# Optimization experiments

Hardware: AMD Instinct MI355X
Metric: run time of the kernel (lower is better)

The kernel has to match this reference:

```python
import jax, jax.numpy as jnp
import numpy as np

# SRU config from the module: 3 layers, highway_bias=0, rescale=True, no layer_norm.
# rescale factor from sru package: sqrt(1 + exp(highway_bias)*2)
SCALE_X = (1.0 + np.exp(0.0) * 2.0) ** 0.5

IMG_DIM, T, HID, NCLS, B = 512, 12, 1024, 51, 2048


def _sru_layer(x, W, vc, b):
    # x: (T, B, d_in); W: (d_in, k*d); vc: (2, d) gate-recurrence vectors; b: (2, d) biases
    Tn, Bn, d_in = x.shape
    d = vc.shape[1]
    k = W.shape[1] // d  # 4 if d_in != d else 3
    U = jnp.einsum('tbi,ij->tbj', x, W).reshape(Tn, Bn, k, d)
    u0, u1, u2 = U[:, :, 0], U[:, :, 1], U[:, :, 2]
    resid = U[:, :, 3] if k == 4 else x  # projected residual when dims differ
    vf, vr = vc[0], vc[1]
    bf, br = b[0], b[1]

    def step(c, inp):
        u0t, u1t, u2t, xt = inp
        f = jax.nn.sigmoid(u1t + vf * c + bf)          # forget gate (uses c_{t-1})
        c_new = f * c + (1.0 - f) * u0t                # cell update
        r = jax.nn.sigmoid(u2t + vr * c_new + br)      # reset gate (uses c_t, as in SRU CUDA)
        h = r * jnp.tanh(c_new) + (1.0 - r) * xt * SCALE_X  # highway with rescale
        return c_new, h

    c0 = jnp.zeros((Bn, d), x.dtype)
    c_last, h = jax.lax.scan(step, c0, (u0, u1, u2, resid))
    return h, c_last


def setup_inputs() -> dict:
    key = jax.random.key(0)
    ks = jax.random.split(key, 12)
    inp = {}
    inp['x'] = jax.random.normal(ks[0], (B, T, IMG_DIM), jnp.float32)
    # layer 0: 512 -> 1024, k=4; layers 1,2: 1024 -> 1024, k=3
    inp['W0'] = jax.random.normal(ks[1], (IMG_DIM, 4 * HID), jnp.float32) / np.sqrt(IMG_DIM)
    inp['W1'] = jax.random.normal(ks[2], (HID, 3 * HID), jnp.float32) / np.sqrt(HID)
    inp['W2'] = jax.random.normal(ks[3], (HID, 3 * HID), jnp.float32) / np.sqrt(HID)
    inp['vc0'] = jax.random.normal(ks[4], (2, HID), jnp.float32) * 0.1
    inp['vc1'] = jax.random.normal(ks[5], (2, HID), jnp.float32) * 0.1
    inp['vc2'] = jax.random.normal(ks[6], (2, HID), jnp.float32) * 0.1
    inp['b0'] = jnp.zeros((2, HID), jnp.float32)
    inp['b1'] = jnp.zeros((2, HID), jnp.float32)
    inp['b2'] = jnp.zeros((2, HID), jnp.float32)
    inp['fc_w'] = jax.random.normal(ks[7], (HID, NCLS), jnp.float32) / np.sqrt(HID)
    inp['fc_b'] = jnp.zeros((NCLS,), jnp.float32)
    return inp


def reference(x, W0, W1, W2, vc0, vc1, vc2, b0, b1, b2, fc_w, fc_b):
    h = jnp.transpose(x, (1, 0, 2))  # (T, B, img_dim)
    for W, vc, b in ((W0, vc0, b0), (W1, vc1, b1), (W2, vc2, b2)):
        h, _ = _sru_layer(h, W, vc, b)
    # dropout layers are identity in eval mode
    logits = jnp.einsum('tbh,hc->tbc', h, fc_w) + fc_b  # (T, B, num_class)
    return jnp.mean(logits, axis=0)  # (B, num_class)
```

## Files before the change

### kernel.cpp

```cpp
#include <hip/hip_runtime.h>
#include <math.h>

#define TSTEPS 12
#define BATCH  2048
#define IMG    512
#define HIDN   1024
#define NCLASS 51
#define SCALE_X 1.7320508075688772f

typedef __attribute__((ext_vector_type(8)))  _Float16 f16x8;
typedef __attribute__((ext_vector_type(2)))  _Float16 f16x2;
typedef __attribute__((ext_vector_type(16))) float    f32x16;

__device__ __forceinline__ float sigf(float x) {
    return 1.f / (1.f + __expf(-x));
}

#define VMCNT_IMM(n) (0x0F70 | (n))


template<int TJ, int NCOMP>
__global__ __launch_bounds__(256, 2)
void gemm_sru(const _Float16* __restrict__ A, const _Float16* __restrict__ Bt,
              const _Float16* __restrict__ resid,
              const float* __restrict__ vc, const float* __restrict__ bias,
              _Float16* __restrict__ hout, float* __restrict__ hbar, int K,
              int pcshift) {
    constexpr int BN    = 64 * TJ;
    constexpr int NCH   = BN / NCOMP;
    constexpr int ATILE = 192 * 32;
    constexpr int EPAD  = BN + 8;
    constexpr int EPI   = 96 * EPAD;
    constexpr int HREG  = 96 * NCH;
    constexpr int KTH   = NCH / 16;
    constexpr int PAIRS = NCH / 2;
    constexpr int STG   = 4 * ATILE;
    constexpr int TOT   = STG > (EPI + HREG) ? STG : (EPI + HREG);
    __shared__ __align__(16) _Float16 smem[TOT];

    const int tid  = threadIdx.x;
    const int lane = tid & 63;
    const int w    = tid >> 6;

    const int nbx = gridDim.x;
    const int b   = blockIdx.y * nbx + blockIdx.x;
    const int pc1 = (nbx >> 3) - 1;
    const int xk  = b & 7, s = b >> 3;
    const int bx  = xk + ((s & pc1) << 3);
    const int by  = s >> pcshift;

    const int bm  = by * 192;
    const int KT  = K >> 4;

    const int rt0 = bm >> 5;
    auto stageA = [&](int buf, int k0) {
        const int kt0 = k0 >> 4;
        #pragma unroll
        for (int i = 0; i < 3; ++i) {
            const int L = w * 3 + i, rc = L >> 1, kk = L & 1;
            const _Float16* g = A + ((size_t)(rt0 + rc) * KT + kt0 + kk) * 512 + (lane << 3);
            __builtin_amdgcn_global_load_lds(
                (const __attribute__((address_space(1))) unsigned int*)g,
                (__attribute__((address_space(3))) unsigned int*)(smem + buf * ATILE + L * 512),
                16, 0, 0);
        }
    };

    const int wy32 = (w >> 1) * 3;
    const int wx32 = (w & 1) * TJ;
    const int l5   = lane >> 5;
    const int m32  = lane & 31;

    const _Float16* bglob = Bt + (size_t)(bx * (BN >> 5) + wx32) * KT * 512 + (lane << 3);

    f16x8 bfr[2][2][TJ];
    auto loadB = [&](int k0, int slot) {
        const int kt0 = k0 >> 4;
        #pragma unroll
        for (int ks = 0; ks < 2; ++ks)
            #pragma unroll
            for (int j = 0; j < TJ; ++j)
                bfr[slot][ks][j] = *(const f16x8*)&bglob[((size_t)j * KT + kt0 + ks) * 512];
    };

    f32x16 acc[3][TJ];
    #pragma unroll
    for (int i = 0; i < 3; ++i)
        #pragma unroll
        for (int j = 0; j < TJ; ++j)
            #pragma unroll
            for (int r = 0; r < 16; ++r) acc[i][j][r] = 0.f;

    stageA(0, 0);
    stageA(1, 32);
    loadB(0, 0);

    for (int K0 = 0; K0 < K; K0 += 128) {
        #pragma unroll
        for (int u = 0; u < 4; ++u) {
            const int k0 = K0 + u * 32;
            if (k0 + 32 < K) __builtin_amdgcn_s_waitcnt(VMCNT_IMM(3 + 2 * TJ));
            else             __builtin_amdgcn_s_waitcnt(VMCNT_IMM(2 * TJ));
            __builtin_amdgcn_s_barrier();
            if (k0 + 64 < K) stageA((u + 2) & 3, k0 + 64);
            if (k0 + 32 < K) loadB(k0 + 32, (u + 1) & 1);

            const _Float16* la = smem + u * ATILE;
            #pragma unroll
            for (int ks = 0; ks < 2; ++ks) {
                f16x8 a[3];
                #pragma unroll
                for (int i = 0; i < 3; ++i)
                    a[i] = *(const f16x8*)&la[((wy32 + i) * 2 + ks) * 512 + (lane << 3)];
                #pragma unroll
                for (int i = 0; i < 3; ++i)
                    #pragma unroll
                    for (int j = 0; j < TJ; ++j)
                        acc[i][j] = __builtin_amdgcn_mfma_f32_32x32x16_f16(
                            a[i], bfr[u & 1][ks][j], acc[i][j], 0, 0, 0);
            }
        }
    }

    _Float16 (*uld)[EPAD] = (_Float16 (*)[EPAD])smem;
    _Float16* hreg = smem + EPI;
    const int bl   = tid / PAIRS;
    const int pr   = tid % PAIRS;
    const int gcol = bx * NCH + pr * 2;

    #pragma unroll
    for (int pass = 0; pass < 2; ++pass) {
        __syncthreads();
        if ((w >> 1) == pass) {
            #pragma unroll
            for (int i = 0; i < 3; ++i)
                #pragma unroll
                for (int j = 0; j < TJ; ++j)
                    #pragma unroll
                    for (int r = 0; r < 16; ++r) {
                        const int row = i * 32 + (r & 3) + 8 * (r >> 2) + 4 * l5;
                        uld[row][(wx32 + j) * 32 + m32] = (_Float16)acc[i][j][r];
                    }
        }
        __syncthreads();

        if (tid < 8 * PAIRS) {
            const float2 vf  = *(const float2*)&vc[gcol];
            const float2 vr  = *(const float2*)&vc[HIDN + gcol];
            const float2 bfv = *(const float2*)&bias[gcol];
            const float2 brv = *(const float2*)&bias[HIDN + gcol];
            const int ca = (pr * 2) * NCOMP, cb = (pr * 2 + 1) * NCOMP;

            float c0 = 0.f, c1 = 0.f, s0 = 0.f, s1 = 0.f;
            #pragma unroll
            for (int t = 0; t < TSTEPS; ++t) {
                const int row = bl * 12 + t;
                const float u0a = (float)uld[row][ca + 0];
                const float u1a = (float)uld[row][ca + 1];
                const float u2a = (float)uld[row][ca + 2];
                const float u0b = (float)uld[row][cb + 0];
                const float u1b = (float)uld[row][cb + 1];
                const float u2b = (float)uld[row][cb + 2];
                float xta, xtb;
                if (NCOMP == 4) {
                    xta = (float)uld[row][ca + 3];
                    xtb = (float)uld[row][cb + 3];
                } else {
                    const int grow = bm + pass * 96 + row;
                    const size_t gran = ((size_t)(grow >> 5) * KT + (gcol >> 4)) * 512
                                      + (size_t)((grow & 31) + ((gcol >> 3) & 1) * 32) * 8
                                      + (gcol & 7);
                    const f16x2 xv = *(const f16x2*)&resid[gran];
                    xta = (float)xv[0]; xtb = (float)xv[1];
                }

                const float f0 = sigf(u1a + vf.x * c0 + bfv.x);
                c0 = f0 * c0 + (1.f - f0) * u0a;
                const float r0_ = sigf(u2a + vr.x * c0 + brv.x);
                const float th0 = 2.f * sigf(2.f * c0) - 1.f;
                const float hv0 = r0_ * th0 + (1.f - r0_) * xta * SCALE_X;

                const float f1 = sigf(u1b + vf.y * c1 + bfv.y);
                c1 = f1 * c1 + (1.f - f1) * u0b;
                const float r1_ = sigf(u2b + vr.y * c1 + brv.y);
                const float th1 = 2.f * sigf(2.f * c1) - 1.f;
                const float hv1 = r1_ * th1 + (1.f - r1_) * xtb * SCALE_X;

                if (hout) {
                    const int rtl  = row >> 5;
                    const int ktl  = pr >> 3;
                    const int lloc = (row & 31) + ((pr >> 2) & 1) * 32;
                    f16x2 hv = { (_Float16)hv0, (_Float16)hv1 };
                    *(f16x2*)&hreg[(rtl * KTH + ktl) * 512 + lloc * 8 + (pr & 3) * 2] = hv;
                }
                s0 += hv0; s1 += hv1;
            }
            if (hbar) {
                const int gb = bm / 12 + pass * 8 + bl;
                *(float2*)&hbar[(size_t)gb * HIDN + gcol] =
                    make_float2(s0 * (1.f / TSTEPS), s1 * (1.f / TSTEPS));
            }
        }

        if (hout) {
            __syncthreads();
            const int rtg0 = (bm + pass * 96) >> 5;
            for (int g = tid; g < HREG / 8; g += 256) {
                const int c = g >> 6, l = g & 63;
                const f16x8 v = *(const f16x8*)&hreg[c * 512 + l * 8];
                const int rtl = c / KTH, ktl = c % KTH;
                const size_t gc = (size_t)(rtg0 + rtl) * 64 + bx * KTH + ktl;
                *(f16x8*)&hout[gc * 512 + l * 8] = v;
            }
        }
    }
}

template<int NC>
__global__ __launch_bounds__(256)
void wsplit_t(const float* __restrict__ W, _Float16* __restrict__ Wt, int K) {
    __shared__ _Float16 tile[32][132];
    const int N  = NC * 1024;
    const int KT = K >> 4;
    const int rt = blockIdx.x, kc = blockIdx.y;

    const int nl = threadIdx.x & 31;
    const int kl = threadIdx.x >> 5;
    const int np = rt * 32 + nl;
    const int h  = np / NC, comp = np - h * NC;
    const int n  = comp * 1024 + h;
    #pragma unroll
    for (int kk = 0; kk < 16; ++kk) {
        const int k = kc * 128 + kl * 16 + kk;
        tile[nl][kl * 16 + kk] = (_Float16)W[(size_t)k * N + n];
    }
    __syncthreads();

    #pragma unroll
    for (int p = 0; p < 2; ++p) {
        const int slot = p * 256 + threadIdx.x;
        const int ktl  = slot >> 6, l = slot & 63;
        f16x8 v;
        #pragma unroll
        for (int j = 0; j < 8; ++j)
            v[j] = tile[l & 31][ktl * 16 + ((l >> 5) << 3) + j];
        const int kt = kc * 8 + ktl;
        *(f16x8*)&Wt[((size_t)rt * KT + kt) * 512 + l * 8] = v;
    }
}

__global__ __launch_bounds__(256)
void esplit(const float* __restrict__ src, _Float16* __restrict__ dst) {
    __shared__ _Float16 tile[32][132];
    const int rt = blockIdx.x, kc = blockIdx.y;
    const int kli = threadIdx.x & 31;
    const int rl  = threadIdx.x >> 5;
    #pragma unroll
    for (int rr = 0; rr < 4; ++rr) {
        const int row = rl * 4 + rr;
        const float4 v = *(const float4*)&src[(size_t)(rt * 32 + row) * 512 + kc * 128 + kli * 4];
        tile[row][kli * 4 + 0] = (_Float16)v.x;
        tile[row][kli * 4 + 1] = (_Float16)v.y;
        tile[row][kli * 4 + 2] = (_Float16)v.z;
        tile[row][kli * 4 + 3] = (_Float16)v.w;
    }
    __syncthreads();

    #pragma unroll
    for (int p = 0; p < 2; ++p) {
        const int slot = p * 256 + threadIdx.x;
        const int ktl  = slot >> 6, l = slot & 63;
        f16x8 v;
        #pragma unroll
        for (int j = 0; j < 8; ++j)
            v[j] = tile[l & 31][ktl * 16 + ((l >> 5) << 3) + j];
        const int kt = kc * 8 + ktl;
        *(f16x8*)&dst[((size_t)rt * 32 + kt) * 512 + l * 8] = v;
    }
}

__global__ __launch_bounds__(64)
void final_fc(const float* __restrict__ hbar, const float* __restrict__ fcw,
              const float* __restrict__ fcb, float* __restrict__ out) {
    __shared__ float hrow[HIDN];
    const int b = blockIdx.x;
    for (int i = threadIdx.x; i < HIDN; i += 64)
        hrow[i] = hbar[(size_t)b * HIDN + i];
    __syncthreads();

    const int c = threadIdx.x;
    if (c < NCLASS) {
        float acc = fcb[c];
        #pragma unroll 8
        for (int k = 0; k < HIDN; ++k)
            acc = fmaf(hrow[k], fcw[(size_t)k * NCLASS + c], acc);
        out[(size_t)b * NCLASS + c] = acc;
    }
}

extern "C" void kernel_launch(void* const* d_in, const int* in_sizes, int n_in,
                              void* d_out, int out_size, void* d_ws, size_t ws_size,
                              hipStream_t stream) {
    const float* x   = (const float*)d_in[0];
    const float* W0  = (const float*)d_in[1];
    const float* W1  = (const float*)d_in[2];
    const float* W2  = (const float*)d_in[3];
    const float* vc0 = (const float*)d_in[4];
    const float* vc1 = (const float*)d_in[5];
    const float* vc2 = (const float*)d_in[6];
    const float* b0  = (const float*)d_in[7];
    const float* b1  = (const float*)d_in[8];
    const float* b2  = (const float*)d_in[9];
    const float* fcw = (const float*)d_in[10];
    const float* fcb = (const float*)d_in[11];
    float* out = (float*)d_out;

    char* ws = (char*)d_ws;
    size_t off = 0;
    auto carve = [&](size_t bytes) { char* p = ws + off; off = (off + bytes + 255) & ~255ull; return p; };

    _Float16* W0t = (_Float16*)carve((size_t)4096 * 512 * 2);
    _Float16* W1t = (_Float16*)carve((size_t)3072 * 1024 * 2);
    _Float16* W2t = (_Float16*)carve((size_t)3072 * 1024 * 2);
    const size_t W_BYTES = off;

    const size_t PER_B = 12ull * 512 * 2 + 2ull * 12 * 1024 * 2 + 1024ull * 4 + 1024;
    int CB = 32;
    if      (W_BYTES + 2048ull * PER_B <= ws_size) CB = 2048;
    else if (W_BYTES + 1024ull * PER_B <= ws_size) CB = 1024;
    else if (W_BYTES +  512ull * PER_B <= ws_size) CB = 512;
    else if (W_BYTES +  256ull * PER_B <= ws_size) CB = 256;
    else if (W_BYTES +  128ull * PER_B <= ws_size) CB = 128;
    else if (W_BYTES +   64ull * PER_B <= ws_size) CB = 64;
    const int MC = CB * TSTEPS;

    _Float16* x16  = (_Float16*)carve((size_t)MC * 512 * 2);
    _Float16* hA16 = (_Float16*)carve((size_t)MC * 1024 * 2);
    _Float16* hB16 = (_Float16*)carve((size_t)MC * 1024 * 2);
    float*    hbar = (float*)carve((size_t)CB * 1024 * 4);

    const dim3 blk256(256);

    wsplit_t<4><<<dim3(4096 / 32, 512 / 128),  blk256, 0, stream>>>(W0, W0t, 512);
    wsplit_t<3><<<dim3(3072 / 32, 1024 / 128), blk256, 0, stream>>>(W1, W1t, 1024);
    wsplit_t<3><<<dim3(3072 / 32, 1024 / 128), blk256, 0, stream>>>(W2, W2t, 1024);

    for (int cb = 0; cb < BATCH / CB; ++cb) {
        const float* xc   = x   + (size_t)cb * CB * TSTEPS * IMG;
        float*       outc = out + (size_t)cb * CB * NCLASS;

        esplit<<<dim3(MC / 32, 4), blk256, 0, stream>>>(xc, x16);
        gemm_sru<2, 4><<<dim3(4096 / 128, MC / 192), blk256, 0, stream>>>(
            x16, W0t, nullptr, vc0, b0, hA16, nullptr, 512, 2);

        gemm_sru<3, 3><<<dim3(3072 / 192, MC / 192), blk256, 0, stream>>>(
            hA16, W1t, hA16, vc1, b1, hB16, nullptr, 1024, 1);

        gemm_sru<3, 3><<<dim3(3072 / 192, MC / 192), blk256, 0, stream>>>(
            hB16, W2t, hB16, vc2, b2, nullptr, hbar, 1024, 1);

        final_fc<<<dim3(CB), dim3(64), 0, stream>>>(hbar, fcw, fcb, outc);
    }
}
```

Measured before the change: 740.8 us.

## Deepen A tile to K=64 per stage with triple-buffered LDS pipeline

Each LDS A stage now covers 64 K-elements instead of 32, and the ring drops from four 32-wide buffers to three 64-wide ones. This halves the number of waitcnt/barrier points per K sweep and gives more MFMA work per barrier. B register fragments are now loaded within the same iteration: one half is fetched just before it is used, and the other half is prefetched for the next step. In exchange, LDS use per block grows, which may affect occupancy. The shorter B prefetch distance and the fixed vmcnt threshold could also expose global-load latency or weaken synchronization near the tail.

```diff
diff --git a/kernel.cpp b/kernel.cpp
--- a/kernel.cpp
+++ b/kernel.cpp
@@ -28,13 +28,13 @@
               int pcshift) {
     constexpr int BN    = 64 * TJ;
     constexpr int NCH   = BN / NCOMP;
-    constexpr int ATILE = 192 * 32;
+    constexpr int ATILE = 192 * 64;
     constexpr int EPAD  = BN + 8;
     constexpr int EPI   = 96 * EPAD;
     constexpr int HREG  = 96 * NCH;
     constexpr int KTH   = NCH / 16;
     constexpr int PAIRS = NCH / 2;
-    constexpr int STG   = 4 * ATILE;
+    constexpr int STG   = 3 * ATILE;
     constexpr int TOT   = STG > (EPI + HREG) ? STG : (EPI + HREG);
     __shared__ __align__(16) _Float16 smem[TOT];
 
@@ -56,8 +56,8 @@
     auto stageA = [&](int buf, int k0) {
         const int kt0 = k0 >> 4;
         #pragma unroll
-        for (int i = 0; i < 3; ++i) {
-            const int L = w * 3 + i, rc = L >> 1, kk = L & 1;
+        for (int i = 0; i < 6; ++i) {
+            const int L = w * 6 + i, rc = L >> 2, kk = L & 3;
             const _Float16* g = A + ((size_t)(rt0 + rc) * KT + kt0 + kk) * 512 + (lane << 3);
             __builtin_amdgcn_global_load_lds(
                 (const __attribute__((address_space(1))) unsigned int*)g,
@@ -91,35 +91,56 @@
             #pragma unroll
             for (int r = 0; r < 16; ++r) acc[i][j][r] = 0.f;
 
+    const int NV = K >> 6;
+
     stageA(0, 0);
-    stageA(1, 32);
+    stageA(1, 64);
     loadB(0, 0);
 
-    for (int K0 = 0; K0 < K; K0 += 128) {
-        #pragma unroll
-        for (int u = 0; u < 4; ++u) {
-            const int k0 = K0 + u * 32;
-            if (k0 + 32 < K) __builtin_amdgcn_s_waitcnt(VMCNT_IMM(3 + 2 * TJ));
-            else             __builtin_amdgcn_s_waitcnt(VMCNT_IMM(2 * TJ));
-            __builtin_amdgcn_s_barrier();
-            if (k0 + 64 < K) stageA((u + 2) & 3, k0 + 64);
-            if (k0 + 32 < K) loadB(k0 + 32, (u + 1) & 1);
-
-            const _Float16* la = smem + u * ATILE;
-            #pragma unroll
-            for (int ks = 0; ks < 2; ++ks) {
-                f16x8 a[3];
+    int rb = 0, sb = 2;
+    for (int v = 0; v < NV; ++v) {
+        const int k0 = v << 6;
+        __builtin_amdgcn_s_waitcnt(VMCNT_IMM(6 + 2 * TJ));
+        __builtin_amdgcn_s_barrier();
+
+        const _Float16* la = smem + rb * ATILE;
+
+        loadB(k0 + 32, 1);
+        __builtin_amdgcn_sched_barrier(0);
+        if (v + 2 < NV) stageA(sb, k0 + 128);
+
+        #pragma unroll
+        for (int ks = 0; ks < 2; ++ks) {
+            f16x8 a[3];
+            #pragma unroll
+            for (int i = 0; i < 3; ++i)
+                a[i] = *(const f16x8*)&la[((wy32 + i) * 4 + ks) * 512 + (lane << 3)];
+            #pragma unroll
+            for (int i = 0; i < 3; ++i)
                 #pragma unroll
-                for (int i = 0; i < 3; ++i)
-                    a[i] = *(const f16x8*)&la[((wy32 + i) * 2 + ks) * 512 + (lane << 3)];
+                for (int j = 0; j < TJ; ++j)
+                    acc[i][j] = __builtin_amdgcn_mfma_f32_32x32x16_f16(
+                        a[i], bfr[0][ks][j], acc[i][j], 0, 0, 0);
+        }
+
+        if (v + 1 < NV) loadB(k0 + 64, 0);
+
+        #pragma unroll
+        for (int ks = 0; ks < 2; ++ks) {
+            f16x8 a[3];
+            #pragma unroll
+            for (int i = 0; i < 3; ++i)
+                a[i] = *(const f16x8*)&la[((wy32 + i) * 4 + 2 + ks) * 512 + (lane << 3)];
+            #pragma unroll
+            for (int i = 0; i < 3; ++i)
                 #pragma unroll
-                for (int i = 0; i < 3; ++i)
-                    #pragma unroll
-                    for (int j = 0; j < TJ; ++j)
-                        acc[i][j] = __builtin_amdgcn_mfma_f32_32x32x16_f16(
-                            a[i], bfr[u & 1][ks][j], acc[i][j], 0, 0, 0);
-            }
-        }
+                for (int j = 0; j < TJ; ++j)
+                    acc[i][j] = __builtin_amdgcn_mfma_f32_32x32x16_f16(
+                        a[i], bfr[1][ks][j], acc[i][j], 0, 0, 0);
+        }
+
+        rb = (rb == 2) ? 0 : rb + 1;
+        sb = (sb == 2) ? 0 : sb + 1;
     }
 
     _Float16 (*uld)[EPAD] = (_Float16 (*)[EPAD])smem;
```

New measurement: 745.6 us. About the same (+0.6%).

## Widen GEMM K-tile to 64 with triple-buffered A and four B register banks

Applied to the files above, without the earlier changes.

Restructures the GEMM main loop to consume 64-wide K slices per step, with three LDS A buffers instead of four 32-wide ones. Each step splits into two MFMA halves. A separate register bank holds the B fragments for each half, and those are prefetched one step ahead. Loads are pinned by sched_barrier and MFMA priority is raised with s_setprio, aiming for fewer barriers per K and better overlap of memory with MFMA. The vmcnt immediate encoding is extended to the high bits because the larger wait counts no longer fit in 4 bits. The tail waitcnt special case is dropped, which risks a race on the final steps.

```diff
diff --git a/kernel.cpp b/kernel.cpp
--- a/kernel.cpp
+++ b/kernel.cpp
@@ -16,7 +16,7 @@
     return 1.f / (1.f + __expf(-x));
 }
 
-#define VMCNT_IMM(n) (0x0F70 | (n))
+#define VMCNT_IMM(n) (0x0F70 | ((n) & 15) | (((n) >> 4) << 14))
 
 
 template<int TJ, int NCOMP>
@@ -28,13 +28,13 @@
               int pcshift) {
     constexpr int BN    = 64 * TJ;
     constexpr int NCH   = BN / NCOMP;
-    constexpr int ATILE = 192 * 32;
+    constexpr int ATILE = 192 * 64;
     constexpr int EPAD  = BN + 8;
     constexpr int EPI   = 96 * EPAD;
     constexpr int HREG  = 96 * NCH;
     constexpr int KTH   = NCH / 16;
     constexpr int PAIRS = NCH / 2;
-    constexpr int STG   = 4 * ATILE;
+    constexpr int STG   = 3 * ATILE;
     constexpr int TOT   = STG > (EPI + HREG) ? STG : (EPI + HREG);
     __shared__ __align__(16) _Float16 smem[TOT];
 
@@ -56,8 +56,8 @@
     auto stageA = [&](int buf, int k0) {
         const int kt0 = k0 >> 4;
         #pragma unroll
-        for (int i = 0; i < 3; ++i) {
-            const int L = w * 3 + i, rc = L >> 1, kk = L & 1;
+        for (int i = 0; i < 6; ++i) {
+            const int L = w * 6 + i, rc = L >> 2, kk = L & 3;
             const _Float16* g = A + ((size_t)(rt0 + rc) * KT + kt0 + kk) * 512 + (lane << 3);
             __builtin_amdgcn_global_load_lds(
                 (const __attribute__((address_space(1))) unsigned int*)g,
@@ -73,15 +73,54 @@
 
     const _Float16* bglob = Bt + (size_t)(bx * (BN >> 5) + wx32) * KT * 512 + (lane << 3);
 
-    f16x8 bfr[2][2][TJ];
-    auto loadB = [&](int k0, int slot) {
-        const int kt0 = k0 >> 4;
-        #pragma unroll
-        for (int ks = 0; ks < 2; ++ks)
-            #pragma unroll
-            for (int j = 0; j < TJ; ++j)
-                bfr[slot][ks][j] = *(const f16x8*)&bglob[((size_t)j * KT + kt0 + ks) * 512];
-    };
+    f16x8 bW[2][TJ], bX[2][TJ], bY[2][TJ], bZ[2][TJ];
+
+#define LOADB(DST, k0v)                                                        \
+    do {                                                                       \
+        const int kt0_ = (k0v) >> 4;                                           \
+        _Pragma("unroll")                                                      \
+        for (int ks = 0; ks < 2; ++ks)                                         \
+            _Pragma("unroll")                                                  \
+            for (int j = 0; j < TJ; ++j)                                       \
+                DST[ks][j] = *(const f16x8*)&bglob[((size_t)j * KT + kt0_ + ks) * 512]; \
+    } while (0)
+
+#define MFMA_HALF(BANK, KSB)                                                   \
+    do {                                                                       \
+        _Pragma("unroll")                                                      \
+        for (int ks = 0; ks < 2; ++ks) {                                       \
+            f16x8 a_[3];                                                       \
+            _Pragma("unroll")                                                  \
+            for (int i = 0; i < 3; ++i)                                        \
+                a_[i] = *(const f16x8*)&la[((wy32 + i) * 4 + (KSB) + ks) * 512 + (lane << 3)]; \
+            _Pragma("unroll")                                                  \
+            for (int i = 0; i < 3; ++i)                                        \
+                _Pragma("unroll")                                              \
+                for (int j = 0; j < TJ; ++j)                                   \
+                    acc[i][j] = __builtin_amdgcn_mfma_f32_32x32x16_f16(        \
+                        a_[i], BANK[ks][j], acc[i][j], 0, 0, 0);               \
+        }                                                                      \
+    } while (0)
+
+#define KSTEP(vv, CONS0, CONS1, FILL0, FILL1)                                  \
+    do {                                                                       \
+        __builtin_amdgcn_s_waitcnt(VMCNT_IMM(6 + 4 * TJ));                     \
+        __builtin_amdgcn_s_barrier();                                          \
+        const _Float16* la = smem + rb * ATILE;                                \
+        if ((vv) + 1 < NV) LOADB(FILL0, ((vv) + 1) << 6);                      \
+        __builtin_amdgcn_sched_barrier(0);                                     \
+        if ((vv) + 2 < NV) stageA(sb, ((vv) + 2) << 6);                        \
+        __builtin_amdgcn_s_setprio(1);                                         \
+        MFMA_HALF(CONS0, 0);                                                   \
+        __builtin_amdgcn_s_setprio(0);                                         \
+        __builtin_amdgcn_s_barrier();                                          \
+        if ((vv) + 1 < NV) LOADB(FILL1, (((vv) + 1) << 6) + 32);               \
+        __builtin_amdgcn_s_setprio(1);                                         \
+        MFMA_HALF(CONS1, 2);                                                   \
+        __builtin_amdgcn_s_setprio(0);                                         \
+        rb = (rb == 2) ? 0 : rb + 1;                                           \
+        sb = (sb == 2) ? 0 : sb + 1;                                           \
+    } while (0)
 
     f32x16 acc[3][TJ];
     #pragma unroll
@@ -91,36 +130,22 @@
             #pragma unroll
             for (int r = 0; r < 16; ++r) acc[i][j][r] = 0.f;
 
+    const int NV = K >> 6;
+
     stageA(0, 0);
-    stageA(1, 32);
-    loadB(0, 0);
-
-    for (int K0 = 0; K0 < K; K0 += 128) {
-        #pragma unroll
-        for (int u = 0; u < 4; ++u) {
-            const int k0 = K0 + u * 32;
-            if (k0 + 32 < K) __builtin_amdgcn_s_waitcnt(VMCNT_IMM(3 + 2 * TJ));
-            else             __builtin_amdgcn_s_waitcnt(VMCNT_IMM(2 * TJ));
-            __builtin_amdgcn_s_barrier();
-            if (k0 + 64 < K) stageA((u + 2) & 3, k0 + 64);
-            if (k0 + 32 < K) loadB(k0 + 32, (u + 1) & 1);
-
-            const _Float16* la = smem + u * ATILE;
-            #pragma unroll
-            for (int ks = 0; ks < 2; ++ks) {
-                f16x8 a[3];
-                #pragma unroll
-                for (int i = 0; i < 3; ++i)
-                    a[i] = *(const f16x8*)&la[((wy32 + i) * 2 + ks) * 512 + (lane << 3)];
-                #pragma unroll
-                for (int i = 0; i < 3; ++i)
-                    #pragma unroll
-                    for (int j = 0; j < TJ; ++j)
-                        acc[i][j] = __builtin_amdgcn_mfma_f32_32x32x16_f16(
-                            a[i], bfr[u & 1][ks][j], acc[i][j], 0, 0, 0);
-            }
-        }
-    }
+    stageA(1, 64);
+    LOADB(bW, 0);
+    LOADB(bX, 32);
+
+    int rb = 0, sb = 2;
+    for (int v = 0; v < NV; v += 2) {
+        KSTEP(v,     bW, bX, bY, bZ);
+        KSTEP(v + 1, bY, bZ, bW, bX);
+    }
+
+#undef KSTEP
+#undef MFMA_HALF
+#undef LOADB
 
     _Float16 (*uld)[EPAD] = (_Float16 (*)[EPAD])smem;
     _Float16* hreg = smem + EPI;
```

New measurement: 1.050 ms. +41.7%, slower.

## Drop LDS staging and software pipeline; load A and B fragments directly from global

Applied to the files above, without the earlier changes.

Removes the 4-stage LDS ring for A tiles (global_load_lds with manual vmcnt waits and barriers) and the double-buffered B register prefetch. Each wave now loads its A and B fragments straight from global memory in a simple unrolled K loop and relies on the compiler for latency hiding. This cuts barriers and shared-memory traffic and lowers LDS usage, but A tiles shared by two waves are now fetched twice from global/L2, and explicit prefetch overlap is lost.

```diff
diff --git a/kernel.cpp b/kernel.cpp
--- a/kernel.cpp
+++ b/kernel.cpp
@@ -15,8 +15,6 @@
 __device__ __forceinline__ float sigf(float x) {
     return 1.f / (1.f + __expf(-x));
 }
-
-#define VMCNT_IMM(n) (0x0F70 | (n))
 
 
 template<int TJ, int NCOMP>
@@ -28,15 +26,12 @@
               int pcshift) {
     constexpr int BN    = 64 * TJ;
     constexpr int NCH   = BN / NCOMP;
-    constexpr int ATILE = 192 * 32;
     constexpr int EPAD  = BN + 8;
     constexpr int EPI   = 96 * EPAD;
     constexpr int HREG  = 96 * NCH;
     constexpr int KTH   = NCH / 16;
     constexpr int PAIRS = NCH / 2;
-    constexpr int STG   = 4 * ATILE;
-    constexpr int TOT   = STG > (EPI + HREG) ? STG : (EPI + HREG);
-    __shared__ __align__(16) _Float16 smem[TOT];
+    __shared__ __align__(16) _Float16 smem[EPI + HREG];
 
     const int tid  = threadIdx.x;
     const int lane = tid & 63;
@@ -51,37 +46,15 @@
 
     const int bm  = by * 192;
     const int KT  = K >> 4;
-
     const int rt0 = bm >> 5;
-    auto stageA = [&](int buf, int k0) {
-        const int kt0 = k0 >> 4;
-        #pragma unroll
-        for (int i = 0; i < 3; ++i) {
-            const int L = w * 3 + i, rc = L >> 1, kk = L & 1;
-            const _Float16* g = A + ((size_t)(rt0 + rc) * KT + kt0 + kk) * 512 + (lane << 3);
-            __builtin_amdgcn_global_load_lds(
-                (const __attribute__((address_space(1))) unsigned int*)g,
-                (__attribute__((address_space(3))) unsigned int*)(smem + buf * ATILE + L * 512),
-                16, 0, 0);
-        }
-    };
 
     const int wy32 = (w >> 1) * 3;
     const int wx32 = (w & 1) * TJ;
     const int l5   = lane >> 5;
     const int m32  = lane & 31;
 
+    const _Float16* aglob = A  + (size_t)(rt0 + wy32) * KT * 512 + (lane << 3);
     const _Float16* bglob = Bt + (size_t)(bx * (BN >> 5) + wx32) * KT * 512 + (lane << 3);
-
-    f16x8 bfr[2][2][TJ];
-    auto loadB = [&](int k0, int slot) {
-        const int kt0 = k0 >> 4;
-        #pragma unroll
-        for (int ks = 0; ks < 2; ++ks)
-            #pragma unroll
-            for (int j = 0; j < TJ; ++j)
-                bfr[slot][ks][j] = *(const f16x8*)&bglob[((size_t)j * KT + kt0 + ks) * 512];
-    };
 
     f32x16 acc[3][TJ];
     #pragma unroll
@@ -91,35 +64,21 @@
             #pragma unroll
             for (int r = 0; r < 16; ++r) acc[i][j][r] = 0.f;
 
-    stageA(0, 0);
-    stageA(1, 32);
-    loadB(0, 0);
-
-    for (int K0 = 0; K0 < K; K0 += 128) {
-        #pragma unroll
-        for (int u = 0; u < 4; ++u) {
-            const int k0 = K0 + u * 32;
-            if (k0 + 32 < K) __builtin_amdgcn_s_waitcnt(VMCNT_IMM(3 + 2 * TJ));
-            else             __builtin_amdgcn_s_waitcnt(VMCNT_IMM(2 * TJ));
-            __builtin_amdgcn_s_barrier();
-            if (k0 + 64 < K) stageA((u + 2) & 3, k0 + 64);
-            if (k0 + 32 < K) loadB(k0 + 32, (u + 1) & 1);
-
-            const _Float16* la = smem + u * ATILE;
+    #pragma unroll 4
+    for (int kt = 0; kt < KT; ++kt) {
+        f16x8 av[3], bv[TJ];
+        #pragma unroll
+        for (int i = 0; i < 3; ++i)
+            av[i] = *(const f16x8*)&aglob[((size_t)i * KT + kt) * 512];
+        #pragma unroll
+        for (int j = 0; j < TJ; ++j)
+            bv[j] = *(const f16x8*)&bglob[((size_t)j * KT + kt) * 512];
+        #pragma unroll
+        for (int i = 0; i < 3; ++i)
             #pragma unroll
-            for (int ks = 0; ks < 2; ++ks) {
-                f16x8 a[3];
-                #pragma unroll
-                for (int i = 0; i < 3; ++i)
-                    a[i] = *(const f16x8*)&la[((wy32 + i) * 2 + ks) * 512 + (lane << 3)];
-                #pragma unroll
-                for (int i = 0; i < 3; ++i)
-                    #pragma unroll
-                    for (int j = 0; j < TJ; ++j)
-                        acc[i][j] = __builtin_amdgcn_mfma_f32_32x32x16_f16(
-                            a[i], bfr[u & 1][ks][j], acc[i][j], 0, 0, 0);
-            }
-        }
+            for (int j = 0; j < TJ; ++j)
+                acc[i][j] = __builtin_amdgcn_mfma_f32_32x32x16_f16(
+                    av[i], bv[j], acc[i][j], 0, 0, 0);
     }
 
     _Float16 (*uld)[EPAD] = (_Float16 (*)[EPAD])smem;
```

Result: slower. 1.023 ms (+38.0%).
